# Kernel tuning notes

Measured on AMD Instinct MI355X. Metric: run time of the kernel, lower is better.

## Reference

```python
import jax, jax.numpy as jnp
import numpy as np

B, N, D = 32, 2048, 512
Q, C = 8, 1024
COMMIT_W = 0.02


def setup_inputs() -> dict:
    key = jax.random.key(0)
    kx, kc = jax.random.split(key)
    x = jax.random.normal(kx, (B, N, D), dtype=jnp.float32)
    codebooks = jax.random.normal(kc, (Q, C, D), dtype=jnp.float32)  # per-quantizer embed tables
    return {"x": x, "codebooks": codebooks}


def _quantize(residual, embed):
    # residual: (B,N,D), embed: (C,D)
    flat = residual.reshape(-1, residual.shape[-1])  # (B*N, D)
    dist = (
        jnp.sum(flat * flat, axis=-1, keepdims=True)
        - 2.0 * (flat @ embed.T)
        + jnp.sum(embed * embed, axis=-1)
    )  # (B*N, C)
    idx = jnp.argmin(dist, axis=-1)  # (B*N,)
    q = embed[idx].reshape(residual.shape)  # codebook gather
    # commitment loss: mse(residual, stopgrad(quantized))
    commit = jnp.mean((jax.lax.stop_gradient(q) - residual) ** 2)
    # straight-through estimator
    q_st = residual + jax.lax.stop_gradient(q - residual)
    return idx.reshape(residual.shape[:-1]), q_st, commit


def reference(x, codebooks):
    residual = x
    quantized_out = jnp.zeros_like(x)
    all_indices = []
    all_losses = []
    for qi in range(Q):
        idx, quantized, commit = _quantize(residual, codebooks[qi])
        residual = residual - jax.lax.stop_gradient(quantized)
        quantized_out = quantized_out + quantized
        all_indices.append(idx)
        all_losses.append(commit * COMMIT_W)
    all_indices = jnp.stack(all_indices, axis=-1)  # (B, N, Q) int
    all_losses = jnp.stack(all_losses, axis=-1)  # (Q,)
    final_commit_loss = jnp.sum(all_losses)
    return quantized_out, all_indices, all_losses, final_commit_loss
```

## Files before the change

kernel.cpp:

```cpp
#include <hip/hip_runtime.h>

#define TOKENS   65536
#define DDIM     512
#define NQ       8
#define NCODES   1024
#define COMMIT_W 0.02

#define MT       32
#define NT       512
#define NBLOCKS  (TOKENS / MT)
#define KSPLIT   384

#define OFF_IDX  ((size_t)TOKENS * DDIM)
#define OFF_LOSS (OFF_IDX + (size_t)TOKENS * NQ)
#define OFF_TOT  (OFF_LOSS + NQ)

typedef _Float16 f16;
typedef _Float16 f16x8 __attribute__((ext_vector_type(8)));
typedef float    f32x4 __attribute__((ext_vector_type(4)));

__device__ __forceinline__ bool better(float d, int i, float bd, int bi) {
  return (d < bd) || (d == bd && i < bi);
}

__device__ __forceinline__ void ins4(float dd, int c, float cd[4], int ci[4]) {
  if (better(dd, c, cd[3], ci[3])) {
    if (better(dd, c, cd[1], ci[1])) {
      if (better(dd, c, cd[0], ci[0])) {
        cd[3]=cd[2]; ci[3]=ci[2]; cd[2]=cd[1]; ci[2]=ci[1];
        cd[1]=cd[0]; ci[1]=ci[0]; cd[0]=dd; ci[0]=c;
      } else {
        cd[3]=cd[2]; ci[3]=ci[2]; cd[2]=cd[1]; ci[2]=ci[1];
        cd[1]=dd; ci[1]=c;
      }
    } else {
      if (better(dd, c, cd[2], ci[2])) { cd[3]=cd[2]; ci[3]=ci[2]; cd[2]=dd; ci[2]=c; }
      else { cd[3]=dd; ci[3]=c; }
    }
  }
}

__device__ __forceinline__ void merge4(float cd[4], int ci[4], const int m) {
  const float b0 = __shfl_xor(cd[0], m, 64), b1 = __shfl_xor(cd[1], m, 64),
              b2 = __shfl_xor(cd[2], m, 64), b3 = __shfl_xor(cd[3], m, 64);
  const int   o0 = __shfl_xor(ci[0], m, 64), o1 = __shfl_xor(ci[1], m, 64),
              o2 = __shfl_xor(ci[2], m, 64), o3 = __shfl_xor(ci[3], m, 64);
  float L0, L1, L2, L3; int M0, M1, M2, M3;
  if (better(b3, o3, cd[0], ci[0])) { L0 = b3; M0 = o3; } else { L0 = cd[0]; M0 = ci[0]; }
  if (better(b2, o2, cd[1], ci[1])) { L1 = b2; M1 = o2; } else { L1 = cd[1]; M1 = ci[1]; }
  if (better(b1, o1, cd[2], ci[2])) { L2 = b1; M2 = o1; } else { L2 = cd[2]; M2 = ci[2]; }
  if (better(b0, o0, cd[3], ci[3])) { L3 = b0; M3 = o0; } else { L3 = cd[3]; M3 = ci[3]; }
  if (better(L2, M2, L0, M0)) { float t=L0; L0=L2; L2=t; int u=M0; M0=M2; M2=u; }
  if (better(L3, M3, L1, M1)) { float t=L1; L1=L3; L3=t; int u=M1; M1=M3; M3=u; }
  if (better(L1, M1, L0, M0)) { float t=L0; L0=L1; L1=t; int u=M0; M0=M1; M1=u; }
  if (better(L3, M3, L2, M2)) { float t=L2; L2=L3; L3=t; int u=M2; M2=M3; M3=u; }
  cd[0]=L0; ci[0]=M0; cd[1]=L1; ci[1]=M1; cd[2]=L2; ci[2]=M2; cd[3]=L3; ci[3]=M3;
}

__device__ __forceinline__ float pw128_row_sq(const float* __restrict__ a) {
  float r0 = __fmul_rn(a[0], a[0]), r1 = __fmul_rn(a[1], a[1]);
  float r2 = __fmul_rn(a[2], a[2]), r3 = __fmul_rn(a[3], a[3]);
  float r4 = __fmul_rn(a[4], a[4]), r5 = __fmul_rn(a[5], a[5]);
  float r6 = __fmul_rn(a[6], a[6]), r7 = __fmul_rn(a[7], a[7]);
  for (int i = 8; i < 128; i += 8) {
    r0 = __fadd_rn(r0, __fmul_rn(a[i + 0], a[i + 0]));
    r1 = __fadd_rn(r1, __fmul_rn(a[i + 1], a[i + 1]));
    r2 = __fadd_rn(r2, __fmul_rn(a[i + 2], a[i + 2]));
    r3 = __fadd_rn(r3, __fmul_rn(a[i + 3], a[i + 3]));
    r4 = __fadd_rn(r4, __fmul_rn(a[i + 4], a[i + 4]));
    r5 = __fadd_rn(r5, __fmul_rn(a[i + 5], a[i + 5]));
    r6 = __fadd_rn(r6, __fmul_rn(a[i + 6], a[i + 6]));
    r7 = __fadd_rn(r7, __fmul_rn(a[i + 7], a[i + 7]));
  }
  return __fadd_rn(__fadd_rn(__fadd_rn(r0, r1), __fadd_rn(r2, r3)),
                   __fadd_rn(__fadd_rn(r4, r5), __fadd_rn(r6, r7)));
}

__global__ void prep_kernel(const float* __restrict__ cb, float* __restrict__ eef) {
  const int code = blockIdx.x * blockDim.x + threadIdx.x;
  if (code < NQ * NCODES) {
    const float* e = cb + (size_t)code * DDIM;
    const float p0 = pw128_row_sq(e), p1 = pw128_row_sq(e + 128);
    const float p2 = pw128_row_sq(e + 256), p3 = pw128_row_sq(e + 384);
    eef[code] = __fadd_rn(__fadd_rn(p0, p1), __fadd_rn(p2, p3));
  }
}

__global__ void cvt_kernel(const float* __restrict__ cb, f16* __restrict__ cbH) {
  const size_t base = ((size_t)blockIdx.x * 256 + threadIdx.x) * 8;
  const float4 v0 = *(const float4*)(cb + base);
  const float4 v1 = *(const float4*)(cb + base + 4);
  f16x8 h;
  h[0] = (f16)v0.x; h[1] = (f16)v0.y; h[2] = (f16)v0.z; h[3] = (f16)v0.w;
  h[4] = (f16)v1.x; h[5] = (f16)v1.y; h[6] = (f16)v1.z; h[7] = (f16)v1.w;
  *(f16x8*)(cbH + base) = h;
}

__global__ void __launch_bounds__(NT, 4)
rvq_main(const float* __restrict__ x, const float* __restrict__ cb,
         const f16* __restrict__ cbH, const float* __restrict__ eef,
         double* __restrict__ lossPart, float* __restrict__ outq,
         float* __restrict__ outidx) {
  __shared__ float  r_t[DDIM * MT];
  __shared__ __align__(16) char smem_u[8192];
  __shared__ float  ee_lds[NCODES];
  __shared__ int    hist[MT][NQ];
  __shared__ double wred[8];

  f16*   ra  = (f16*)smem_u;
  float* wcd = (float*)smem_u;
  int*   wci = (int*)(smem_u + 4096);

  const int tid  = threadIdx.x;
  const int lane = tid & 63;
  const int wv   = tid >> 6;
  const int cbase = wv << 7;
  const int blockTok = blockIdx.x * MT;

  {
    const int tm = tid & 31, kp = tid >> 5;
    const float* xr = x + (size_t)(blockTok + tm) * DDIM;
#pragma unroll
    for (int i = 0; i < 8; ++i) {
      const int d4 = (kp + i * 16) << 2;
      const float4 v = *(const float4*)(xr + d4);
      r_t[(d4 + 0) * MT + tm] = v.x;
      r_t[(d4 + 1) * MT + tm] = v.y;
      r_t[(d4 + 2) * MT + tm] = v.z;
      r_t[(d4 + 3) * MT + tm] = v.w;
    }
  }
  __syncthreads();

  const int la15 = lane & 15;
  const int kg8  = (lane >> 4) << 3;
  const int swz  = (la15 & 7) << 3;

  for (int qi = 0; qi < NQ; ++qi) {
    const float* cbq   = cb  + (size_t)qi * NCODES * DDIM;
    const f16*   cbq16 = cbH + (size_t)qi * NCODES * DDIM;
    const float* enq   = eef + qi * NCODES;

#pragma unroll
    for (int j = 0; j < 2; ++j) ee_lds[tid + j * NT] = enq[tid + j * NT];

    f32x4 acc[8][2];
#pragma unroll
    for (int mt = 0; mt < 8; ++mt) {
      acc[mt][0] = (f32x4){0.f, 0.f, 0.f, 0.f};
      acc[mt][1] = (f32x4){0.f, 0.f, 0.f, 0.f};
    }

    for (int ch = 0; ch < 4; ++ch) {
      __syncthreads();
      {
        const int tok  = tid & 31;
        const int ko   = tid >> 5;
        const int tswz = (tok & 7) << 3;
        const int kl   = ko << 3;
        const int kg   = (ch << 7) + kl;
        f16x8 h;
#pragma unroll
        for (int j = 0; j < 8; ++j) h[j] = (f16)r_t[(kg + j) * MT + tok];
        *(f16x8*)&ra[tok * 128 + (kl ^ tswz)] = h;
      }
      __syncthreads();
#pragma unroll
      for (int s = 0; s < 4; ++s) {
        const int kk = (s << 5) + kg8;
        const f16x8 b0 = *(const f16x8*)&ra[la15 * 128 + (kk ^ swz)];
        const f16x8 b1 = *(const f16x8*)&ra[(la15 + 16) * 128 + (kk ^ swz)];
        const f16* ap = cbq16 + (size_t)(cbase + la15) * DDIM + (ch << 7) + kk;
#pragma unroll
        for (int mt = 0; mt < 8; ++mt) {
          const f16x8 a = *(const f16x8*)(ap + (size_t)(mt << 4) * DDIM);
          acc[mt][0] = __builtin_amdgcn_mfma_f32_16x16x32_f16(a, b0, acc[mt][0], 0, 0, 0);
          acc[mt][1] = __builtin_amdgcn_mfma_f32_16x16x32_f16(a, b1, acc[mt][1], 0, 0, 0);
        }
      }
    }
    __syncthreads();

    float cd0[4], cd1[4]; int ci0[4], ci1[4];
#pragma unroll
    for (int s = 0; s < 4; ++s) {
      cd0[s] = 3.0e38f; ci0[s] = 0x7fffffff;
      cd1[s] = 3.0e38f; ci1[s] = 0x7fffffff;
    }
    const int rbase = cbase + ((lane >> 4) << 2);
#pragma unroll
    for (int mt = 0; mt < 8; ++mt) {
#pragma unroll
      for (int r = 0; r < 4; ++r) {
        const int code = rbase + (mt << 4) + r;
        const float eb = ee_lds[code];
        ins4(fmaf(-2.0f, acc[mt][0][r], eb), code, cd0, ci0);
        ins4(fmaf(-2.0f, acc[mt][1][r], eb), code, cd1, ci1);
      }
    }
    merge4(cd0, ci0, 16); merge4(cd0, ci0, 32);
    merge4(cd1, ci1, 16); merge4(cd1, ci1, 32);

    if (lane < 16) {
      const int w32 = wv << 5;
#pragma unroll
      for (int s = 0; s < 4; ++s) {
        wcd[(w32 + lane) * 4 + s]      = cd0[s];
        wci[(w32 + lane) * 4 + s]      = ci0[s];
        wcd[(w32 + lane + 16) * 4 + s] = cd1[s];
        wci[(w32 + lane + 16) * 4 + s] = ci1[s];
      }
    }
    __syncthreads();

    if (tid < 128) {
      const int tok4 = tid >> 2, cnd = tid & 3;
      float fd[4]; int fi[4];
#pragma unroll
      for (int s = 0; s < 4; ++s) { fd[s] = 3.0e38f; fi[s] = 0x7fffffff; }
      for (int w2 = 0; w2 < 8; ++w2) {
#pragma unroll
        for (int s = 0; s < 4; ++s) {
          const int e = ((w2 << 5) + tok4) * 4 + s;
          ins4(wcd[e], wci[e], fd, fi);
        }
      }
      const int cme = fi[cnd];

      float blk;
      {
        const int kb = cnd * 128;
        float a[8];
#pragma unroll
        for (int j = 0; j < 8; ++j) {
          const float v = r_t[(kb + j) * MT + tok4];
          a[j] = __fmul_rn(v, v);
        }
        for (int i = 8; i < 128; i += 8) {
#pragma unroll
          for (int j = 0; j < 8; ++j) {
            const float v = r_t[(kb + i + j) * MT + tok4];
            a[j] = __fadd_rn(a[j], __fmul_rn(v, v));
          }
        }
        blk = __fadd_rn(__fadd_rn(__fadd_rn(a[0], a[1]), __fadd_rn(a[2], a[3])),
                        __fadd_rn(__fadd_rn(a[4], a[5]), __fadd_rn(a[6], a[7])));
      }
      const float pw256 = __fadd_rn(blk, __shfl_xor(blk, 1, 64));
      const float rr    = __fadd_rn(pw256, __shfl_xor(pw256, 2, 64));

      const float* ep = cbq + (size_t)cme * DDIM;
      float Sa = 0.f, Sb = 0.f;
      for (int kb = 0; kb < DDIM; kb += 8) {
        const float4 e0 = *(const float4*)(ep + kb);
        const float4 e1 = *(const float4*)(ep + kb + 4);
        const float ev[8] = {e0.x, e0.y, e0.z, e0.w, e1.x, e1.y, e1.z, e1.w};
        float rv[8];
#pragma unroll
        for (int j = 0; j < 8; ++j) rv[j] = r_t[(kb + j) * MT + tok4];
        if (kb < KSPLIT) {
#pragma unroll
          for (int j = 0; j < 8; ++j) Sa = __fmaf_rn(rv[j], ev[j], Sa);
        } else {
#pragma unroll
          for (int j = 0; j < 8; ++j) Sb = __fmaf_rn(rv[j], ev[j], Sb);
        }
      }
      const float cross = __fadd_rn(Sa, Sb);
      const float u = __fsub_rn(rr, __fmul_rn(2.0f, cross));
      float dW = __fadd_rn(u, enq[cme]);
      int   cW = cme;
#pragma unroll
      for (int m = 1; m <= 2; m <<= 1) {
        const float od = __shfl_xor(dW, m, 64);
        const int   oc = __shfl_xor(cW, m, 64);
        if (better(od, oc, dW, cW)) { dW = od; cW = oc; }
      }
      if (cnd == 0) {
        hist[tok4][qi] = cW;
        outidx[(size_t)(blockTok + tok4) * NQ + qi] = (float)cW;
      }
    }
    __syncthreads();

    {
      const int utok = tid & 31;
      const int ks   = tid >> 5;
      const int wc = hist[utok][qi];
      const float* ew = cbq + (size_t)wc * DDIM + (ks << 5);
      double lssq = 0.0;
#pragma unroll
      for (int i = 0; i < 8; ++i) {
        const float4 qv = *(const float4*)(ew + (i << 2));
        const float qa[4] = {qv.x, qv.y, qv.z, qv.w};
        const int k0 = (ks << 5) + (i << 2);
#pragma unroll
        for (int e = 0; e < 4; ++e) {
          const float r  = r_t[(k0 + e) * MT + utok];
          const float a  = __fsub_rn(qa[e], r);
          const float qs = __fadd_rn(r, a);
          const float rn = __fsub_rn(r, qs);
          r_t[(k0 + e) * MT + utok] = rn;
          lssq += (double)a * (double)a;
        }
      }
#pragma unroll
      for (int off = 32; off; off >>= 1) lssq += __shfl_down(lssq, off, 64);
      if ((tid & 63) == 0) wred[tid >> 6] = lssq;
    }
    __syncthreads();
    if (tid == 0) {
      double s = 0.0;
#pragma unroll
      for (int w = 0; w < 8; ++w) s += wred[w];
      lossPart[(size_t)blockIdx.x * NQ + qi] = s;
    }
  }

  {
    const int tokR = tid >> 4;
    const int part = tid & 15;
#pragma unroll
    for (int i = 0; i < 8; ++i) {
      const int d4 = (part + i * 16) << 2;
      const float4 xv = *(const float4*)(x + (size_t)(blockTok + tokR) * DDIM + d4);
      float r[4]  = {xv.x, xv.y, xv.z, xv.w};
      float qa[4] = {0.f, 0.f, 0.f, 0.f};
#pragma unroll
      for (int j = 0; j < NQ; ++j) {
        const int hj = hist[tokR][j];
        const float4 ev = *(const float4*)(cb + ((size_t)j * NCODES + hj) * DDIM + d4);
        const float qv[4] = {ev.x, ev.y, ev.z, ev.w};
#pragma unroll
        for (int e = 0; e < 4; ++e) {
          const float a  = __fsub_rn(qv[e], r[e]);
          const float qs = __fadd_rn(r[e], a);
          r[e]  = __fsub_rn(r[e], qs);
          qa[e] = __fadd_rn(qa[e], qs);
        }
      }
      float4 pk; pk.x = qa[0]; pk.y = qa[1]; pk.z = qa[2]; pk.w = qa[3];
      *(float4*)(outq + (size_t)(blockTok + tokR) * DDIM + d4) = pk;
    }
  }
}

__global__ void loss_fin(const double* __restrict__ lossPart,
                         float* __restrict__ outLoss,
                         float* __restrict__ outTot) {
  __shared__ double sq[NQ];
  const int tid = threadIdx.x;
  const int qi  = tid >> 5, l32 = tid & 31;
  double s = 0.0;
  for (int b = l32; b < NBLOCKS; b += 32) s += lossPart[(size_t)b * NQ + qi];
#pragma unroll
  for (int off = 16; off; off >>= 1) s += __shfl_down(s, off, 32);
  if (l32 == 0) sq[qi] = s;
  __syncthreads();
  if (tid == 0) {
    double tot = 0.0;
    for (int q = 0; q < NQ; ++q) {
      const double v = sq[q] * (COMMIT_W / ((double)TOKENS * (double)DDIM));
      outLoss[q] = (float)v;
      tot += v;
    }
    *outTot = (float)tot;
  }
}

extern "C" void kernel_launch(void* const* d_in, const int* in_sizes, int n_in,
                              void* d_out, int out_size, void* d_ws, size_t ws_size,
                              hipStream_t stream) {
  const float* x  = (const float*)d_in[0];
  const float* cb = (const float*)d_in[1];
  float* out = (float*)d_out;

  float*  eef      = (float*)((char*)d_ws + 256);
  f16*    cbH      = (f16*)((char*)d_ws + 65536);
  double* lossPart = (double*)((char*)d_ws + 65536 + (size_t)NQ * NCODES * DDIM * 2);

  prep_kernel<<<dim3(32), dim3(256), 0, stream>>>(cb, eef);
  cvt_kernel<<<dim3(2048), dim3(256), 0, stream>>>(cb, cbH);
  rvq_main<<<dim3(NBLOCKS), dim3(NT), 0, stream>>>(x, cb, cbH, eef, lossPart,
                                                   out, out + OFF_IDX);
  loss_fin<<<dim3(1), dim3(256), 0, stream>>>(lossPart, out + OFF_LOSS, out + OFF_TOT);
}
```

Before: 3.495 ms.

## Pre-pack fp16 codebook in MFMA fragment order and swizzle residual LDS layout

The conversion kernel now writes the fp16 codebook already arranged in MFMA A-fragment order, so each wave's codebook load in the distance GEMM becomes one contiguous 1 KB read instead of strided 16-byte rows. The transposed residual tile in shared memory gets an XOR swizzle on the token index, to reduce bank conflicts for column-wise accesses. The exact re-scoring dot product is also software-pipelined, prefetching the next codebook and residual chunk. The risks are extra index arithmetic and more register pressure under the 4-waves launch bound.

```diff
diff --git a/kernel.cpp b/kernel.cpp
--- a/kernel.cpp
+++ b/kernel.cpp
@@ -21,6 +21,10 @@
 
 __device__ __forceinline__ bool better(float d, int i, float bd, int bi) {
   return (d < bd) || (d == bd && i < bi);
+}
+
+__device__ __forceinline__ int rtIdx(int k, int tok) {
+  return (k << 5) + ((tok ^ k ^ (k >> 3)) & 31);
 }
 
 __device__ __forceinline__ void ins4(float dd, int c, float cd[4], int ci[4]) {
@@ -86,19 +90,27 @@
   }
 }
 
-__global__ void cvt_kernel(const float* __restrict__ cb, f16* __restrict__ cbH) {
-  const size_t base = ((size_t)blockIdx.x * 256 + threadIdx.x) * 8;
-  const float4 v0 = *(const float4*)(cb + base);
-  const float4 v1 = *(const float4*)(cb + base + 4);
+__global__ void cvt_kernel(const float* __restrict__ cb, f16* __restrict__ cbP) {
+  const int t    = blockIdx.x * 256 + threadIdx.x;
+  const int lane = t & 63;
+  const int s    = (t >> 6) & 3;
+  const int gt   = (t >> 8) & 63;
+  const int ch   = (t >> 14) & 3;
+  const int qi   = t >> 16;
+  const int code = (gt << 4) + (lane & 15);
+  const int k    = (ch << 7) + (s << 5) + (((lane >> 4) & 3) << 3);
+  const float* src = cb + (size_t)(qi * NCODES + code) * DDIM + k;
+  const float4 v0 = *(const float4*)(src);
+  const float4 v1 = *(const float4*)(src + 4);
   f16x8 h;
   h[0] = (f16)v0.x; h[1] = (f16)v0.y; h[2] = (f16)v0.z; h[3] = (f16)v0.w;
   h[4] = (f16)v1.x; h[5] = (f16)v1.y; h[6] = (f16)v1.z; h[7] = (f16)v1.w;
-  *(f16x8*)(cbH + base) = h;
+  *(f16x8*)(cbP + (size_t)t * 8) = h;
 }
 
 __global__ void __launch_bounds__(NT, 4)
 rvq_main(const float* __restrict__ x, const float* __restrict__ cb,
-         const f16* __restrict__ cbH, const float* __restrict__ eef,
+         const f16* __restrict__ cbP, const float* __restrict__ eef,
          double* __restrict__ lossPart, float* __restrict__ outq,
          float* __restrict__ outidx) {
   __shared__ float  r_t[DDIM * MT];
@@ -124,10 +136,10 @@
     for (int i = 0; i < 8; ++i) {
       const int d4 = (kp + i * 16) << 2;
       const float4 v = *(const float4*)(xr + d4);
-      r_t[(d4 + 0) * MT + tm] = v.x;
-      r_t[(d4 + 1) * MT + tm] = v.y;
-      r_t[(d4 + 2) * MT + tm] = v.z;
-      r_t[(d4 + 3) * MT + tm] = v.w;
+      r_t[rtIdx(d4 + 0, tm)] = v.x;
+      r_t[rtIdx(d4 + 1, tm)] = v.y;
+      r_t[rtIdx(d4 + 2, tm)] = v.z;
+      r_t[rtIdx(d4 + 3, tm)] = v.w;
     }
   }
   __syncthreads();
@@ -137,9 +149,8 @@
   const int swz  = (la15 & 7) << 3;
 
   for (int qi = 0; qi < NQ; ++qi) {
-    const float* cbq   = cb  + (size_t)qi * NCODES * DDIM;
-    const f16*   cbq16 = cbH + (size_t)qi * NCODES * DDIM;
-    const float* enq   = eef + qi * NCODES;
+    const float* cbq = cb  + (size_t)qi * NCODES * DDIM;
+    const float* enq = eef + qi * NCODES;
 
 #pragma unroll
     for (int j = 0; j < 2; ++j) ee_lds[tid + j * NT] = enq[tid + j * NT];
@@ -161,7 +172,7 @@
         const int kg   = (ch << 7) + kl;
         f16x8 h;
 #pragma unroll
-        for (int j = 0; j < 8; ++j) h[j] = (f16)r_t[(kg + j) * MT + tok];
+        for (int j = 0; j < 8; ++j) h[j] = (f16)r_t[rtIdx(kg + j, tok)];
         *(f16x8*)&ra[tok * 128 + (kl ^ tswz)] = h;
       }
       __syncthreads();
@@ -170,10 +181,11 @@
         const int kk = (s << 5) + kg8;
         const f16x8 b0 = *(const f16x8*)&ra[la15 * 128 + (kk ^ swz)];
         const f16x8 b1 = *(const f16x8*)&ra[(la15 + 16) * 128 + (kk ^ swz)];
-        const f16* ap = cbq16 + (size_t)(cbase + la15) * DDIM + (ch << 7) + kk;
+        const f16* ap = cbP + ((((size_t)(qi << 2) + ch) * 64 + (cbase >> 4)) * 4 + s) * 512
+                            + (size_t)lane * 8;
 #pragma unroll
         for (int mt = 0; mt < 8; ++mt) {
-          const f16x8 a = *(const f16x8*)(ap + (size_t)(mt << 4) * DDIM);
+          const f16x8 a = *(const f16x8*)(ap + (size_t)mt * 2048);
           acc[mt][0] = __builtin_amdgcn_mfma_f32_16x16x32_f16(a, b0, acc[mt][0], 0, 0, 0);
           acc[mt][1] = __builtin_amdgcn_mfma_f32_16x16x32_f16(a, b1, acc[mt][1], 0, 0, 0);
         }
@@ -233,13 +245,13 @@
         float a[8];
 #pragma unroll
         for (int j = 0; j < 8; ++j) {
-          const float v = r_t[(kb + j) * MT + tok4];
+          const float v = r_t[rtIdx(kb + j, tok4)];
           a[j] = __fmul_rn(v, v);
         }
         for (int i = 8; i < 128; i += 8) {
 #pragma unroll
           for (int j = 0; j < 8; ++j) {
-            const float v = r_t[(kb + i + j) * MT + tok4];
+            const float v = r_t[rtIdx(kb + i + j, tok4)];
             a[j] = __fadd_rn(a[j], __fmul_rn(v, v));
           }
         }
@@ -250,14 +262,20 @@
       const float rr    = __fadd_rn(pw256, __shfl_xor(pw256, 2, 64));
 
       const float* ep = cbq + (size_t)cme * DDIM;
+      float4 e0 = *(const float4*)(ep);
+      float4 e1 = *(const float4*)(ep + 4);
+      float rv[8];
+#pragma unroll
+      for (int j = 0; j < 8; ++j) rv[j] = r_t[rtIdx(j, tok4)];
       float Sa = 0.f, Sb = 0.f;
       for (int kb = 0; kb < DDIM; kb += 8) {
-        const float4 e0 = *(const float4*)(ep + kb);
-        const float4 e1 = *(const float4*)(ep + kb + 4);
+        const int kn = (kb + 8 < DDIM) ? (kb + 8) : kb;
+        const float4 p0 = *(const float4*)(ep + kn);
+        const float4 p1 = *(const float4*)(ep + kn + 4);
+        float nv[8];
+#pragma unroll
+        for (int j = 0; j < 8; ++j) nv[j] = r_t[rtIdx(kn + j, tok4)];
         const float ev[8] = {e0.x, e0.y, e0.z, e0.w, e1.x, e1.y, e1.z, e1.w};
-        float rv[8];
-#pragma unroll
-        for (int j = 0; j < 8; ++j) rv[j] = r_t[(kb + j) * MT + tok4];
         if (kb < KSPLIT) {
 #pragma unroll
           for (int j = 0; j < 8; ++j) Sa = __fmaf_rn(rv[j], ev[j], Sa);
@@ -265,6 +283,9 @@
 #pragma unroll
           for (int j = 0; j < 8; ++j) Sb = __fmaf_rn(rv[j], ev[j], Sb);
         }
+#pragma unroll
+        for (int j = 0; j < 8; ++j) rv[j] = nv[j];
+        e0 = p0; e1 = p1;
       }
       const float cross = __fadd_rn(Sa, Sb);
       const float u = __fsub_rn(rr, __fmul_rn(2.0f, cross));
@@ -296,11 +317,12 @@
         const int k0 = (ks << 5) + (i << 2);
 #pragma unroll
         for (int e = 0; e < 4; ++e) {
-          const float r  = r_t[(k0 + e) * MT + utok];
+          const int ri = rtIdx(k0 + e, utok);
+          const float r  = r_t[ri];
           const float a  = __fsub_rn(qa[e], r);
           const float qs = __fadd_rn(r, a);
           const float rn = __fsub_rn(r, qs);
-          r_t[(k0 + e) * MT + utok] = rn;
+          r_t[ri] = rn;
           lssq += (double)a * (double)a;
         }
       }
@@ -376,12 +398,12 @@
   float* out = (float*)d_out;
 
   float*  eef      = (float*)((char*)d_ws + 256);
-  f16*    cbH      = (f16*)((char*)d_ws + 65536);
+  f16*    cbP      = (f16*)((char*)d_ws + 65536);
   double* lossPart = (double*)((char*)d_ws + 65536 + (size_t)NQ * NCODES * DDIM * 2);
 
   prep_kernel<<<dim3(32), dim3(256), 0, stream>>>(cb, eef);
-  cvt_kernel<<<dim3(2048), dim3(256), 0, stream>>>(cb, cbH);
-  rvq_main<<<dim3(NBLOCKS), dim3(NT), 0, stream>>>(x, cb, cbH, eef, lossPart,
+  cvt_kernel<<<dim3(2048), dim3(256), 0, stream>>>(cb, cbP);
+  rvq_main<<<dim3(NBLOCKS), dim3(NT), 0, stream>>>(x, cb, cbP, eef, lossPart,
                                                    out, out + OFF_IDX);
   loss_fin<<<dim3(1), dim3(256), 0, stream>>>(lossPart, out + OFF_LOSS, out + OFF_TOT);
 }
```

Result: slower. 4.562 ms (+30.5%).

## Software-pipeline MFMA operand loads, swizzle residual LDS layout, prefetch rescoring loads

Applied to the files above, without the earlier changes.

Reorganizes the MFMA inner loop so the next group's codebook fragments and LDS B-operands are loaded while the current group's MFMAs run, hiding global load latency. The transposed residual buffer in LDS gets an XOR swizzle on the token index to reduce bank conflicts on column-wise accesses. The exact-rescoring dot product prefetches codebook rows and residual values one stage ahead, and the final reconstruction hoists histogram reads into registers. The extra in-flight registers may raise VGPR pressure under the 4-wave launch bound and could cause spills.

```diff
diff --git a/kernel.cpp b/kernel.cpp
--- a/kernel.cpp
+++ b/kernel.cpp
@@ -21,6 +21,10 @@
 
 __device__ __forceinline__ bool better(float d, int i, float bd, int bi) {
   return (d < bd) || (d == bd && i < bi);
+}
+
+__device__ __forceinline__ int rtIdx(int k, int tok) {
+  return (k << 5) + ((tok ^ k ^ (k >> 3)) & 31);
 }
 
 __device__ __forceinline__ void ins4(float dd, int c, float cd[4], int ci[4]) {
@@ -96,6 +100,27 @@
   *(f16x8*)(cbH + base) = h;
 }
 
+#define RSTAGE(E0, E1, KC)                                                    \
+  {                                                                           \
+    const int knx = ((KC) + 8 < DDIM) ? (KC) + 8 : (KC);                      \
+    float rvn[8];                                                             \
+    _Pragma("unroll")                                                         \
+    for (int j = 0; j < 8; ++j) rvn[j] = r_t[rtIdx(knx + j, tok4)];           \
+    const float ev[8] = {E0.x, E0.y, E0.z, E0.w, E1.x, E1.y, E1.z, E1.w};     \
+    if ((KC) < KSPLIT) {                                                      \
+      _Pragma("unroll")                                                       \
+      for (int j = 0; j < 8; ++j) Sa = __fmaf_rn(rvc[j], ev[j], Sa);          \
+    } else {                                                                  \
+      _Pragma("unroll")                                                       \
+      for (int j = 0; j < 8; ++j) Sb = __fmaf_rn(rvc[j], ev[j], Sb);          \
+    }                                                                         \
+    const int knr = ((KC) + 32 < DDIM) ? (KC) + 32 : (KC);                    \
+    E0 = *(const float4*)(ep + knr);                                          \
+    E1 = *(const float4*)(ep + knr + 4);                                      \
+    _Pragma("unroll")                                                         \
+    for (int j = 0; j < 8; ++j) rvc[j] = rvn[j];                              \
+  }
+
 __global__ void __launch_bounds__(NT, 4)
 rvq_main(const float* __restrict__ x, const float* __restrict__ cb,
          const f16* __restrict__ cbH, const float* __restrict__ eef,
@@ -124,10 +149,10 @@
     for (int i = 0; i < 8; ++i) {
       const int d4 = (kp + i * 16) << 2;
       const float4 v = *(const float4*)(xr + d4);
-      r_t[(d4 + 0) * MT + tm] = v.x;
-      r_t[(d4 + 1) * MT + tm] = v.y;
-      r_t[(d4 + 2) * MT + tm] = v.z;
-      r_t[(d4 + 3) * MT + tm] = v.w;
+      r_t[rtIdx(d4 + 0, tm)] = v.x;
+      r_t[rtIdx(d4 + 1, tm)] = v.y;
+      r_t[rtIdx(d4 + 2, tm)] = v.z;
+      r_t[rtIdx(d4 + 3, tm)] = v.w;
     }
   }
   __syncthreads();
@@ -161,21 +186,50 @@
         const int kg   = (ch << 7) + kl;
         f16x8 h;
 #pragma unroll
-        for (int j = 0; j < 8; ++j) h[j] = (f16)r_t[(kg + j) * MT + tok];
+        for (int j = 0; j < 8; ++j) h[j] = (f16)r_t[rtIdx(kg + j, tok)];
         *(f16x8*)&ra[tok * 128 + (kl ^ tswz)] = h;
       }
       __syncthreads();
-#pragma unroll
-      for (int s = 0; s < 4; ++s) {
-        const int kk = (s << 5) + kg8;
-        const f16x8 b0 = *(const f16x8*)&ra[la15 * 128 + (kk ^ swz)];
-        const f16x8 b1 = *(const f16x8*)&ra[(la15 + 16) * 128 + (kk ^ swz)];
-        const f16* ap = cbq16 + (size_t)(cbase + la15) * DDIM + (ch << 7) + kk;
-#pragma unroll
-        for (int mt = 0; mt < 8; ++mt) {
-          const f16x8 a = *(const f16x8*)(ap + (size_t)(mt << 4) * DDIM);
-          acc[mt][0] = __builtin_amdgcn_mfma_f32_16x16x32_f16(a, b0, acc[mt][0], 0, 0, 0);
-          acc[mt][1] = __builtin_amdgcn_mfma_f32_16x16x32_f16(a, b1, acc[mt][1], 0, 0, 0);
+
+      const f16* apBase = cbq16 + (size_t)(cbase + la15) * DDIM + (ch << 7);
+      f16x8 bc0 = *(const f16x8*)&ra[la15 * 128 + (kg8 ^ swz)];
+      f16x8 bc1 = *(const f16x8*)&ra[(la15 + 16) * 128 + (kg8 ^ swz)];
+      f16x8 a0 = *(const f16x8*)(apBase + kg8 + (size_t)0 * 16 * DDIM);
+      f16x8 a1 = *(const f16x8*)(apBase + kg8 + (size_t)1 * 16 * DDIM);
+      f16x8 a2 = *(const f16x8*)(apBase + kg8 + (size_t)2 * 16 * DDIM);
+      f16x8 a3 = *(const f16x8*)(apBase + kg8 + (size_t)3 * 16 * DDIM);
+
+#pragma unroll
+      for (int g = 0; g < 8; ++g) {
+        const int s  = g >> 1;
+        const int mb = (g & 1) << 2;
+        f16x8 n0, n1, n2, n3, nb0, nb1;
+        if (g < 7) {
+          const int gn = g + 1;
+          const int sn = gn >> 1, mbn = (gn & 1) << 2;
+          const int kkn = (sn << 5) + kg8;
+          if ((gn & 1) == 0) {
+            nb0 = *(const f16x8*)&ra[la15 * 128 + (kkn ^ swz)];
+            nb1 = *(const f16x8*)&ra[(la15 + 16) * 128 + (kkn ^ swz)];
+          }
+          const f16* apn = apBase + kkn;
+          n0 = *(const f16x8*)(apn + (size_t)(mbn + 0) * 16 * DDIM);
+          n1 = *(const f16x8*)(apn + (size_t)(mbn + 1) * 16 * DDIM);
+          n2 = *(const f16x8*)(apn + (size_t)(mbn + 2) * 16 * DDIM);
+          n3 = *(const f16x8*)(apn + (size_t)(mbn + 3) * 16 * DDIM);
+        }
+        (void)s;
+        acc[mb + 0][0] = __builtin_amdgcn_mfma_f32_16x16x32_f16(a0, bc0, acc[mb + 0][0], 0, 0, 0);
+        acc[mb + 0][1] = __builtin_amdgcn_mfma_f32_16x16x32_f16(a0, bc1, acc[mb + 0][1], 0, 0, 0);
+        acc[mb + 1][0] = __builtin_amdgcn_mfma_f32_16x16x32_f16(a1, bc0, acc[mb + 1][0], 0, 0, 0);
+        acc[mb + 1][1] = __builtin_amdgcn_mfma_f32_16x16x32_f16(a1, bc1, acc[mb + 1][1], 0, 0, 0);
+        acc[mb + 2][0] = __builtin_amdgcn_mfma_f32_16x16x32_f16(a2, bc0, acc[mb + 2][0], 0, 0, 0);
+        acc[mb + 2][1] = __builtin_amdgcn_mfma_f32_16x16x32_f16(a2, bc1, acc[mb + 2][1], 0, 0, 0);
+        acc[mb + 3][0] = __builtin_amdgcn_mfma_f32_16x16x32_f16(a3, bc0, acc[mb + 3][0], 0, 0, 0);
+        acc[mb + 3][1] = __builtin_amdgcn_mfma_f32_16x16x32_f16(a3, bc1, acc[mb + 3][1], 0, 0, 0);
+        if (g < 7) {
+          a0 = n0; a1 = n1; a2 = n2; a3 = n3;
+          if (((g + 1) & 1) == 0) { bc0 = nb0; bc1 = nb1; }
         }
       }
     }
@@ -226,6 +280,12 @@
         }
       }
       const int cme = fi[cnd];
+      const float eeC = enq[cme];
+      const float* ep = cbq + (size_t)cme * DDIM;
+      float4 eA0 = *(const float4*)(ep +  0), eA1 = *(const float4*)(ep +  4);
+      float4 eB0 = *(const float4*)(ep +  8), eB1 = *(const float4*)(ep + 12);
+      float4 eC0 = *(const float4*)(ep + 16), eC1 = *(const float4*)(ep + 20);
+      float4 eD0 = *(const float4*)(ep + 24), eD1 = *(const float4*)(ep + 28);
 
       float blk;
       {
@@ -233,13 +293,13 @@
         float a[8];
 #pragma unroll
         for (int j = 0; j < 8; ++j) {
-          const float v = r_t[(kb + j) * MT + tok4];
+          const float v = r_t[rtIdx(kb + j, tok4)];
           a[j] = __fmul_rn(v, v);
         }
         for (int i = 8; i < 128; i += 8) {
 #pragma unroll
           for (int j = 0; j < 8; ++j) {
-            const float v = r_t[(kb + i + j) * MT + tok4];
+            const float v = r_t[rtIdx(kb + i + j, tok4)];
             a[j] = __fadd_rn(a[j], __fmul_rn(v, v));
           }
         }
@@ -249,26 +309,19 @@
       const float pw256 = __fadd_rn(blk, __shfl_xor(blk, 1, 64));
       const float rr    = __fadd_rn(pw256, __shfl_xor(pw256, 2, 64));
 
-      const float* ep = cbq + (size_t)cme * DDIM;
+      float rvc[8];
+#pragma unroll
+      for (int j = 0; j < 8; ++j) rvc[j] = r_t[rtIdx(j, tok4)];
       float Sa = 0.f, Sb = 0.f;
-      for (int kb = 0; kb < DDIM; kb += 8) {
-        const float4 e0 = *(const float4*)(ep + kb);
-        const float4 e1 = *(const float4*)(ep + kb + 4);
-        const float ev[8] = {e0.x, e0.y, e0.z, e0.w, e1.x, e1.y, e1.z, e1.w};
-        float rv[8];
-#pragma unroll
-        for (int j = 0; j < 8; ++j) rv[j] = r_t[(kb + j) * MT + tok4];
-        if (kb < KSPLIT) {
-#pragma unroll
-          for (int j = 0; j < 8; ++j) Sa = __fmaf_rn(rv[j], ev[j], Sa);
-        } else {
-#pragma unroll
-          for (int j = 0; j < 8; ++j) Sb = __fmaf_rn(rv[j], ev[j], Sb);
-        }
+      for (int kb = 0; kb < DDIM; kb += 32) {
+        RSTAGE(eA0, eA1, kb + 0)
+        RSTAGE(eB0, eB1, kb + 8)
+        RSTAGE(eC0, eC1, kb + 16)
+        RSTAGE(eD0, eD1, kb + 24)
       }
       const float cross = __fadd_rn(Sa, Sb);
       const float u = __fsub_rn(rr, __fmul_rn(2.0f, cross));
-      float dW = __fadd_rn(u, enq[cme]);
+      float dW = __fadd_rn(u, eeC);
       int   cW = cme;
 #pragma unroll
       for (int m = 1; m <= 2; m <<= 1) {
@@ -296,11 +349,12 @@
         const int k0 = (ks << 5) + (i << 2);
 #pragma unroll
         for (int e = 0; e < 4; ++e) {
-          const float r  = r_t[(k0 + e) * MT + utok];
+          const int ri = rtIdx(k0 + e, utok);
+          const float r  = r_t[ri];
           const float a  = __fsub_rn(qa[e], r);
           const float qs = __fadd_rn(r, a);
           const float rn = __fsub_rn(r, qs);
-          r_t[(k0 + e) * MT + utok] = rn;
+          r_t[ri] = rn;
           lssq += (double)a * (double)a;
         }
       }
@@ -320,6 +374,9 @@
   {
     const int tokR = tid >> 4;
     const int part = tid & 15;
+    int hj[NQ];
+#pragma unroll
+    for (int j = 0; j < NQ; ++j) hj[j] = hist[tokR][j];
 #pragma unroll
     for (int i = 0; i < 8; ++i) {
       const int d4 = (part + i * 16) << 2;
@@ -328,8 +385,7 @@
       float qa[4] = {0.f, 0.f, 0.f, 0.f};
 #pragma unroll
       for (int j = 0; j < NQ; ++j) {
-        const int hj = hist[tokR][j];
-        const float4 ev = *(const float4*)(cb + ((size_t)j * NCODES + hj) * DDIM + d4);
+        const float4 ev = *(const float4*)(cb + ((size_t)j * NCODES + hj[j]) * DDIM + d4);
         const float qv[4] = {ev.x, ev.y, ev.z, ev.w};
 #pragma unroll
         for (int e = 0; e < 4; ++e) {
```

New measurement: 5.612 ms. +60.6%, slower.

## Double token tile to 64 per block with 1024 threads and swizzled residual LDS

Applied to the files above, without the earlier changes.

Raises tokens per block from 32 to 64 and threads from 512 to 1024, so each of 16 waves covers 64 codes across 4 token subtiles. Each codebook fp16 fragment loaded from global memory now feeds four MFMAs instead of two, halving codebook traffic per token. The residual LDS layout gets an XOR swizzle to avoid bank conflicts, and candidate indices are stored as bytes to fit the larger reduction buffer. The cost is 128KB+ of LDS per block and more accumulator registers, which limits occupancy to one block per CU.

```diff
diff --git a/kernel.cpp b/kernel.cpp
--- a/kernel.cpp
+++ b/kernel.cpp
@@ -6,8 +6,8 @@
 #define NCODES   1024
 #define COMMIT_W 0.02
 
-#define MT       32
-#define NT       512
+#define MT       64
+#define NT       1024
 #define NBLOCKS  (TOKENS / MT)
 #define KSPLIT   384
 
@@ -21,6 +21,10 @@
 
 __device__ __forceinline__ bool better(float d, int i, float bd, int bi) {
   return (d < bd) || (d == bd && i < bi);
+}
+
+__device__ __forceinline__ int rtIdx(int k, int tok) {
+  return (k << 6) + ((tok ^ k ^ (k >> 3)) & 63);
 }
 
 __device__ __forceinline__ void ins4(float dd, int c, float cd[4], int ci[4]) {
@@ -102,32 +106,32 @@
          double* __restrict__ lossPart, float* __restrict__ outq,
          float* __restrict__ outidx) {
   __shared__ float  r_t[DDIM * MT];
-  __shared__ __align__(16) char smem_u[8192];
+  __shared__ __align__(16) char smem_u[20480];
   __shared__ float  ee_lds[NCODES];
   __shared__ int    hist[MT][NQ];
-  __shared__ double wred[8];
-
-  f16*   ra  = (f16*)smem_u;
-  float* wcd = (float*)smem_u;
-  int*   wci = (int*)(smem_u + 4096);
+  __shared__ double wred[16];
+
+  f16*           ra   = (f16*)smem_u;
+  float*         wcd  = (float*)smem_u;
+  unsigned char* wci8 = (unsigned char*)(smem_u + 16384);
 
   const int tid  = threadIdx.x;
   const int lane = tid & 63;
   const int wv   = tid >> 6;
-  const int cbase = wv << 7;
+  const int cbase = wv << 6;
   const int blockTok = blockIdx.x * MT;
 
   {
-    const int tm = tid & 31, kp = tid >> 5;
+    const int tm = tid >> 4, part = tid & 15;
     const float* xr = x + (size_t)(blockTok + tm) * DDIM;
 #pragma unroll
     for (int i = 0; i < 8; ++i) {
-      const int d4 = (kp + i * 16) << 2;
+      const int d4 = (part + i * 16) << 2;
       const float4 v = *(const float4*)(xr + d4);
-      r_t[(d4 + 0) * MT + tm] = v.x;
-      r_t[(d4 + 1) * MT + tm] = v.y;
-      r_t[(d4 + 2) * MT + tm] = v.z;
-      r_t[(d4 + 3) * MT + tm] = v.w;
+      r_t[rtIdx(d4 + 0, tm)] = v.x;
+      r_t[rtIdx(d4 + 1, tm)] = v.y;
+      r_t[rtIdx(d4 + 2, tm)] = v.z;
+      r_t[rtIdx(d4 + 3, tm)] = v.w;
     }
   }
   __syncthreads();
@@ -141,88 +145,94 @@
     const f16*   cbq16 = cbH + (size_t)qi * NCODES * DDIM;
     const float* enq   = eef + qi * NCODES;
 
-#pragma unroll
-    for (int j = 0; j < 2; ++j) ee_lds[tid + j * NT] = enq[tid + j * NT];
-
-    f32x4 acc[8][2];
-#pragma unroll
-    for (int mt = 0; mt < 8; ++mt) {
-      acc[mt][0] = (f32x4){0.f, 0.f, 0.f, 0.f};
-      acc[mt][1] = (f32x4){0.f, 0.f, 0.f, 0.f};
-    }
+    ee_lds[tid] = enq[tid];
+
+    f32x4 acc[4][4];
+#pragma unroll
+    for (int mt = 0; mt < 4; ++mt)
+#pragma unroll
+      for (int nt = 0; nt < 4; ++nt) acc[mt][nt] = (f32x4){0.f, 0.f, 0.f, 0.f};
 
     for (int ch = 0; ch < 4; ++ch) {
       __syncthreads();
       {
-        const int tok  = tid & 31;
-        const int ko   = tid >> 5;
+        const int tok  = tid & 63;
+        const int ko   = tid >> 6;
         const int tswz = (tok & 7) << 3;
         const int kl   = ko << 3;
         const int kg   = (ch << 7) + kl;
         f16x8 h;
 #pragma unroll
-        for (int j = 0; j < 8; ++j) h[j] = (f16)r_t[(kg + j) * MT + tok];
+        for (int j = 0; j < 8; ++j) h[j] = (f16)r_t[rtIdx(kg + j, tok)];
         *(f16x8*)&ra[tok * 128 + (kl ^ tswz)] = h;
       }
       __syncthreads();
 #pragma unroll
       for (int s = 0; s < 4; ++s) {
         const int kk = (s << 5) + kg8;
-        const f16x8 b0 = *(const f16x8*)&ra[la15 * 128 + (kk ^ swz)];
-        const f16x8 b1 = *(const f16x8*)&ra[(la15 + 16) * 128 + (kk ^ swz)];
+        f16x8 b[4];
+#pragma unroll
+        for (int nt = 0; nt < 4; ++nt)
+          b[nt] = *(const f16x8*)&ra[(la15 + (nt << 4)) * 128 + (kk ^ swz)];
         const f16* ap = cbq16 + (size_t)(cbase + la15) * DDIM + (ch << 7) + kk;
 #pragma unroll
-        for (int mt = 0; mt < 8; ++mt) {
+        for (int mt = 0; mt < 4; ++mt) {
           const f16x8 a = *(const f16x8*)(ap + (size_t)(mt << 4) * DDIM);
-          acc[mt][0] = __builtin_amdgcn_mfma_f32_16x16x32_f16(a, b0, acc[mt][0], 0, 0, 0);
-          acc[mt][1] = __builtin_amdgcn_mfma_f32_16x16x32_f16(a, b1, acc[mt][1], 0, 0, 0);
+#pragma unroll
+          for (int nt = 0; nt < 4; ++nt)
+            acc[mt][nt] = __builtin_amdgcn_mfma_f32_16x16x32_f16(a, b[nt], acc[mt][nt], 0, 0, 0);
         }
       }
     }
     __syncthreads();
 
-    float cd0[4], cd1[4]; int ci0[4], ci1[4];
-#pragma unroll
-    for (int s = 0; s < 4; ++s) {
-      cd0[s] = 3.0e38f; ci0[s] = 0x7fffffff;
-      cd1[s] = 3.0e38f; ci1[s] = 0x7fffffff;
-    }
-    const int rbase = cbase + ((lane >> 4) << 2);
-#pragma unroll
-    for (int mt = 0; mt < 8; ++mt) {
-#pragma unroll
-      for (int r = 0; r < 4; ++r) {
-        const int code = rbase + (mt << 4) + r;
-        const float eb = ee_lds[code];
-        ins4(fmaf(-2.0f, acc[mt][0][r], eb), code, cd0, ci0);
-        ins4(fmaf(-2.0f, acc[mt][1][r], eb), code, cd1, ci1);
-      }
-    }
-    merge4(cd0, ci0, 16); merge4(cd0, ci0, 32);
-    merge4(cd1, ci1, 16); merge4(cd1, ci1, 32);
-
-    if (lane < 16) {
-      const int w32 = wv << 5;
-#pragma unroll
-      for (int s = 0; s < 4; ++s) {
-        wcd[(w32 + lane) * 4 + s]      = cd0[s];
-        wci[(w32 + lane) * 4 + s]      = ci0[s];
-        wcd[(w32 + lane + 16) * 4 + s] = cd1[s];
-        wci[(w32 + lane + 16) * 4 + s] = ci1[s];
+    {
+      float cd[4][4]; int ci[4][4];
+#pragma unroll
+      for (int nt = 0; nt < 4; ++nt)
+#pragma unroll
+        for (int s = 0; s < 4; ++s) { cd[nt][s] = 3.0e38f; ci[nt][s] = 0x7fffffff; }
+      const int rbase = cbase + ((lane >> 4) << 2);
+#pragma unroll
+      for (int mt = 0; mt < 4; ++mt) {
+#pragma unroll
+        for (int r = 0; r < 4; ++r) {
+          const int code = rbase + (mt << 4) + r;
+          const float eb = ee_lds[code];
+#pragma unroll
+          for (int nt = 0; nt < 4; ++nt)
+            ins4(fmaf(-2.0f, acc[mt][nt][r], eb), code, cd[nt], ci[nt]);
+        }
+      }
+#pragma unroll
+      for (int nt = 0; nt < 4; ++nt) {
+        merge4(cd[nt], ci[nt], 16); merge4(cd[nt], ci[nt], 32);
+      }
+      if (lane < 16) {
+        const int w64 = wv << 6;
+#pragma unroll
+        for (int nt = 0; nt < 4; ++nt) {
+          const int t = w64 + (nt << 4) + lane;
+#pragma unroll
+          for (int s = 0; s < 4; ++s) {
+            wcd[t * 4 + s]  = cd[nt][s];
+            wci8[t * 4 + s] = (unsigned char)(ci[nt][s] - cbase);
+          }
+        }
       }
     }
     __syncthreads();
 
-    if (tid < 128) {
+    if (tid < 4 * MT) {
       const int tok4 = tid >> 2, cnd = tid & 3;
       float fd[4]; int fi[4];
 #pragma unroll
       for (int s = 0; s < 4; ++s) { fd[s] = 3.0e38f; fi[s] = 0x7fffffff; }
-      for (int w2 = 0; w2 < 8; ++w2) {
+      for (int w2 = 0; w2 < 16; ++w2) {
 #pragma unroll
         for (int s = 0; s < 4; ++s) {
-          const int e = ((w2 << 5) + tok4) * 4 + s;
-          ins4(wcd[e], wci[e], fd, fi);
+          const int e = ((w2 << 6) + tok4) * 4 + s;
+          ins4(wcd[e], (w2 << 6) + (int)wci8[e], fd, fi);
         }
       }
       const int cme = fi[cnd];
@@ -233,13 +243,13 @@
         float a[8];
 #pragma unroll
         for (int j = 0; j < 8; ++j) {
-          const float v = r_t[(kb + j) * MT + tok4];
+          const float v = r_t[rtIdx(kb + j, tok4)];
           a[j] = __fmul_rn(v, v);
         }
         for (int i = 8; i < 128; i += 8) {
 #pragma unroll
           for (int j = 0; j < 8; ++j) {
-            const float v = r_t[(kb + i + j) * MT + tok4];
+            const float v = r_t[rtIdx(kb + i + j, tok4)];
             a[j] = __fadd_rn(a[j], __fmul_rn(v, v));
           }
         }
@@ -257,7 +267,7 @@
         const float ev[8] = {e0.x, e0.y, e0.z, e0.w, e1.x, e1.y, e1.z, e1.w};
         float rv[8];
 #pragma unroll
-        for (int j = 0; j < 8; ++j) rv[j] = r_t[(kb + j) * MT + tok4];
+        for (int j = 0; j < 8; ++j) rv[j] = r_t[rtIdx(kb + j, tok4)];
         if (kb < KSPLIT) {
 #pragma unroll
           for (int j = 0; j < 8; ++j) Sa = __fmaf_rn(rv[j], ev[j], Sa);
@@ -284,8 +294,8 @@
     __syncthreads();
 
     {
-      const int utok = tid & 31;
-      const int ks   = tid >> 5;
+      const int utok = tid & 63;
+      const int ks   = tid >> 6;
       const int wc = hist[utok][qi];
       const float* ew = cbq + (size_t)wc * DDIM + (ks << 5);
       double lssq = 0.0;
@@ -296,11 +306,12 @@
         const int k0 = (ks << 5) + (i << 2);
 #pragma unroll
         for (int e = 0; e < 4; ++e) {
-          const float r  = r_t[(k0 + e) * MT + utok];
+          const int ri = rtIdx(k0 + e, utok);
+          const float r  = r_t[ri];
           const float a  = __fsub_rn(qa[e], r);
           const float qs = __fadd_rn(r, a);
           const float rn = __fsub_rn(r, qs);
-          r_t[(k0 + e) * MT + utok] = rn;
+          r_t[ri] = rn;
           lssq += (double)a * (double)a;
         }
       }
@@ -312,7 +323,7 @@
     if (tid == 0) {
       double s = 0.0;
 #pragma unroll
-      for (int w = 0; w < 8; ++w) s += wred[w];
+      for (int w = 0; w < 16; ++w) s += wred[w];
       lossPart[(size_t)blockIdx.x * NQ + qi] = s;
     }
   }
@@ -320,6 +331,9 @@
   {
     const int tokR = tid >> 4;
     const int part = tid & 15;
+    int hj[NQ];
+#pragma unroll
+    for (int j = 0; j < NQ; ++j) hj[j] = hist[tokR][j];
 #pragma unroll
     for (int i = 0; i < 8; ++i) {
       const int d4 = (part + i * 16) << 2;
@@ -328,8 +342,7 @@
       float qa[4] = {0.f, 0.f, 0.f, 0.f};
 #pragma unroll
       for (int j = 0; j < NQ; ++j) {
-        const int hj = hist[tokR][j];
-        const float4 ev = *(const float4*)(cb + ((size_t)j * NCODES + hj) * DDIM + d4);
+        const float4 ev = *(const float4*)(cb + ((size_t)j * NCODES + hj[j]) * DDIM + d4);
         const float qv[4] = {ev.x, ev.y, ev.z, ev.w};
 #pragma unroll
         for (int e = 0; e < 4; ++e) {
```

Result: slower. 4.827 ms (+38.1%).
